# Optimization experiments

Measured on AMD Instinct MI355X. Metric: run time of the kernel, lower is better.

## Reference

```python
import jax, jax.numpy as jnp
import numpy as np

MODEL_DIMS = 2048
BATCH, SEQ = 4, 4096
NFREQ = MODEL_DIMS // 2 + 1  # rfft spectrum length


def setup_inputs() -> dict:
    key = jax.random.key(0)
    k1, k2, k3, k4 = jax.random.split(key, 4)
    x = jax.random.normal(k1, (BATCH, SEQ, MODEL_DIMS), dtype=jnp.float32)
    queries = jax.random.normal(k2, (1, 1, NFREQ), dtype=jnp.float32)
    keyvalues = jax.random.normal(k3, (1, 1, NFREQ), dtype=jnp.float32)
    # torch nn.Linear(model_dims, model_dims, bias=False): weight is [out, in]
    w_out = jax.random.normal(k4, (MODEL_DIMS, MODEL_DIMS), dtype=jnp.float32) * (MODEL_DIMS ** -0.5)
    return {"x": x, "queries": queries, "keyvalues": keyvalues, "w_out": w_out}


def reference(x, queries, keyvalues, w_out):
    # hrr.fft = rfft over feature dim -> complex64 [B, S, NFREQ]
    xhat = jnp.fft.rfft(x, axis=-1)
    q = xhat * queries            # real spectral params broadcast-multiply
    kv = xhat * keyvalues
    kv = jnp.cumsum(kv, axis=1)   # causal prefix sum over sequence
    qv = q * kv
    values_hat = jnp.fft.irfft(qv, n=x.shape[-1], axis=-1)  # back to real [B, S, D]
    # torch Linear: y = x @ W^T
    return jnp.einsum('bsd,ed->bse', values_hat, w_out)
```

## Files before the change

kernel.cpp:

```cpp
#include <hip/hip_runtime.h>
#include <hip/hip_bf16.h>
#include <stdint.h>

#define BATCH 4
#define SEQ   4096
#define DIM   2048
#define NFREQ 1025
#define NCPLX 1024
#define ROWS  (BATCH*SEQ)

#define SCH  16
#define NSC  (SEQ/SCH)
#define NSCG 16
#define NGRP (NSC/NSCG)

#define SPEC_STRIDE 257

typedef __bf16 bf16x8 __attribute__((ext_vector_type(8)));
typedef float  f32x4  __attribute__((ext_vector_type(4)));

__device__ __forceinline__ int drev4(int n) {
  return ((n&3)<<8) | (((n>>2)&3)<<6) | (((n>>4)&3)<<4) | (((n>>6)&3)<<2) | ((n>>8)&3);
}
#define ZI(i) ((i) + ((i)>>4))

__device__ __forceinline__ float2 cmulf(float2 a, float2 b) {
  return make_float2(a.x*b.x - a.y*b.y, a.x*b.y + a.y*b.x);
}

__device__ __forceinline__ unsigned short f2bf(float f) {
  union { float f; unsigned u; } v; v.f = f;
  unsigned r = v.u + 0x7fffu + ((v.u >> 16) & 1u);
  return (unsigned short)(r >> 16);
}
__device__ __forceinline__ unsigned packbf(float2 v) {
  return (unsigned)f2bf(v.x) | ((unsigned)f2bf(v.y) << 16);
}
__device__ __forceinline__ float2 unpackbf(unsigned u) {
  union { unsigned u; float f; } a, b;
  a.u = u << 16; b.u = u & 0xffff0000u;
  return make_float2(a.f, b.f);
}

template<int INV>
__device__ __forceinline__ void fft_stages_tw(float2* z, int tid, const float2* tw1) {
  {
    int b4 = tid*4;
    float2 x0=z[ZI(b4)], x1=z[ZI(b4+1)], x2=z[ZI(b4+2)], x3=z[ZI(b4+3)];
    float2 a = make_float2(x0.x+x2.x, x0.y+x2.y), b = make_float2(x0.x-x2.x, x0.y-x2.y);
    float2 c = make_float2(x1.x+x3.x, x1.y+x3.y), d = make_float2(x1.x-x3.x, x1.y-x3.y);
    z[ZI(b4)]   = make_float2(a.x+c.x, a.y+c.y);
    z[ZI(b4+2)] = make_float2(a.x-c.x, a.y-c.y);
    if (!INV) { z[ZI(b4+1)] = make_float2(b.x+d.y, b.y-d.x);
                z[ZI(b4+3)] = make_float2(b.x-d.y, b.y+d.x); }
    else      { z[ZI(b4+1)] = make_float2(b.x-d.y, b.y+d.x);
                z[ZI(b4+3)] = make_float2(b.x+d.y, b.y-d.x); }
  }
  __syncthreads();
#pragma unroll
  for (int s = 0; s < 4; ++s) {
    const int lq = 2 + 2*s;
    const int q  = 1 << lq;
    int j = tid & (q-1), g = tid >> lq;
    int base = (g << (lq+2)) + j;
    float2 w1 = tw1[s]; if (INV) w1.y = -w1.y;
    float2 w2 = cmulf(w1, w1), w3 = cmulf(w2, w1);
    float2 x0 = z[ZI(base)];
    float2 x1 = cmulf(z[ZI(base+q)],   w1);
    float2 x2 = cmulf(z[ZI(base+2*q)], w2);
    float2 x3 = cmulf(z[ZI(base+3*q)], w3);
    float2 a = make_float2(x0.x+x2.x, x0.y+x2.y), b = make_float2(x0.x-x2.x, x0.y-x2.y);
    float2 c = make_float2(x1.x+x3.x, x1.y+x3.y), d = make_float2(x1.x-x3.x, x1.y-x3.y);
    z[ZI(base)]     = make_float2(a.x+c.x, a.y+c.y);
    z[ZI(base+2*q)] = make_float2(a.x-c.x, a.y-c.y);
    if (!INV) { z[ZI(base+q)]   = make_float2(b.x+d.y, b.y-d.x);
                z[ZI(base+3*q)] = make_float2(b.x-d.y, b.y+d.x); }
    else      { z[ZI(base+q)]   = make_float2(b.x-d.y, b.y+d.x);
                z[ZI(base+3*q)] = make_float2(b.x+d.y, b.y-d.x); }
    __syncthreads();
  }
}

__device__ __forceinline__ void make_tw1(int tid, float2* tw1) {
#pragma unroll
  for (int s = 0; s < 4; ++s) {
    const int lq = 2 + 2*s;
    const int q  = 1 << lq;
    int j = tid & (q-1);
    float ang = -6.2831853071795864769f * (float)j / (float)(4*q);
    float sw, cw; __sincosf(ang, &sw, &cw);
    tw1[s] = make_float2(cw, sw);
  }
}

__global__ __launch_bounds__(256) void fwd_wfft(const float* __restrict__ x,
                                                const float* __restrict__ w,
                                                const float* __restrict__ kvs,
                                                uint4* __restrict__ spec,
                                                float2* __restrict__ partial,
                                                unsigned short* __restrict__ H) {
  __shared__ float2 z[ZI(1023)+2];
  __shared__ __align__(16) unsigned short hrow[2048];
  const int tid = threadIdx.x;

  float2 tw1[4];
  make_tw1(tid, tw1);
  const int kA = tid, kB = tid + 256;
  int id0 = ZI(drev4(2*tid)),     id1 = ZI(drev4(2*tid+1));
  int id2 = ZI(drev4(2*tid+512)), id3 = ZI(drev4(2*tid+513));

  if (blockIdx.x >= BATCH*NSC) {
    const int e = blockIdx.x - BATCH*NSC;
    float swA, cwA, swB, cwB;
    __sincosf(-3.14159265358979323846f * (float)kA / 1024.0f, &swA, &cwA);
    __sincosf(-3.14159265358979323846f * (float)kB / 1024.0f, &swB, &cwB);
    const float* wr = w + (size_t)e * DIM;
    float4 c0 = ((const float4*)wr)[tid];
    float4 c1 = ((const float4*)wr)[tid + 256];
    z[id0] = make_float2(c0.x, c0.y); z[id1] = make_float2(c0.z, c0.w);
    z[id2] = make_float2(c1.x, c1.y); z[id3] = make_float2(c1.z, c1.w);
    __syncthreads();
    fft_stages_tw<0>(z, tid, tw1);
    float2 ZkA = z[ZI(kA)], ZnA = z[ZI((NCPLX - kA) & (NCPLX-1))];
    float2 ZkB = z[ZI(kB)], ZnB = z[ZI(768 - tid)];
    float Er = 0.5f*(ZkA.x + ZnA.x), Ei = 0.5f*(ZkA.y - ZnA.y);
    float dr = 0.5f*(ZkA.x - ZnA.x), di = 0.5f*(ZkA.y + ZnA.y);
    float2 vA  = make_float2( Er + cwA*di + swA*dr,  Ei + swA*di - cwA*dr);
    float2 vAp = make_float2( Er - cwA*di - swA*dr, -Ei + swA*di - cwA*dr);
    float Fr = 0.5f*(ZkB.x + ZnB.x), Fi = 0.5f*(ZkB.y - ZnB.y);
    float er = 0.5f*(ZkB.x - ZnB.x), ei = 0.5f*(ZkB.y + ZnB.y);
    float2 vB  = make_float2( Fr + cwB*ei + swB*er,  Fi + swB*ei - cwB*er);
    float2 vBp = make_float2( Fr - cwB*ei - swB*er, -Fi + swB*ei - cwB*er);
    const float invN = 1.0f/2048.0f, twoN = 2.0f/2048.0f;
    float aA  = (tid == 0) ? invN : twoN;
    hrow[tid]        = f2bf(aA   * vA.x);
    hrow[1024 - tid] = f2bf(aA   * vAp.x);
    hrow[256 + tid]  = f2bf(twoN * vB.x);
    hrow[768 - tid]  = f2bf(twoN * vBp.x);
    if (tid) {
      hrow[1024 + tid] = f2bf(twoN * vA.y);
      hrow[2048 - tid] = f2bf(twoN * vAp.y);
    }
    hrow[1280 + tid] = f2bf(twoN * vB.y);
    hrow[1792 - tid] = f2bf(twoN * vBp.y);
    if (tid == 0) {
      float2 Z5 = z[ZI(512)];
      hrow[512]  = f2bf(twoN * Z5.x);
      hrow[1536] = f2bf(twoN * (-Z5.y));
    }
    __syncthreads();
    ((uint4*)(H + (size_t)e * DIM))[tid] = ((const uint4*)hrow)[tid];
    return;
  }

  const int sc = blockIdx.x & (NSC-1), b = blockIdx.x >> 8;
  float swA, cwA, swB, cwB;
  __sincosf(-3.14159265358979323846f * (float)kA / 1024.0f, &swA, &cwA);
  __sincosf(-3.14159265358979323846f * (float)kB / 1024.0f, &swB, &cwB);

  float2 sA={0,0}, sAp={0,0}, sB={0,0}, sBp={0,0}, s5={0,0};

  const size_t row0 = (size_t)b*SEQ + (size_t)sc*SCH;
  const float* xrow = x + row0*DIM;
  float4 c0 = ((const float4*)xrow)[tid];
  float4 c1 = ((const float4*)xrow)[tid + 256];

  for (int s = 0; s < SCH; ++s) {
    float4 n0f, n1f;
    if (s+1 < SCH) {
      const float* nx = xrow + (size_t)(s+1)*DIM;
      n0f = ((const float4*)nx)[tid]; n1f = ((const float4*)nx)[tid + 256];
    }
    z[id0] = make_float2(c0.x, c0.y); z[id1] = make_float2(c0.z, c0.w);
    z[id2] = make_float2(c1.x, c1.y); z[id3] = make_float2(c1.z, c1.w);
    __syncthreads();
    fft_stages_tw<0>(z, tid, tw1);
    float2 ZkA = z[ZI(kA)], ZnA = z[ZI((NCPLX - kA) & (NCPLX-1))];
    float2 ZkB = z[ZI(kB)], ZnB = z[ZI(768 - tid)];
    float Er = 0.5f*(ZkA.x + ZnA.x), Ei = 0.5f*(ZkA.y - ZnA.y);
    float dr = 0.5f*(ZkA.x - ZnA.x), di = 0.5f*(ZkA.y + ZnA.y);
    float2 vA  = make_float2( Er + cwA*di + swA*dr,  Ei + swA*di - cwA*dr);
    float2 vAp = make_float2( Er - cwA*di - swA*dr, -Ei + swA*di - cwA*dr);
    float Fr = 0.5f*(ZkB.x + ZnB.x), Fi = 0.5f*(ZkB.y - ZnB.y);
    float er = 0.5f*(ZkB.x - ZnB.x), ei = 0.5f*(ZkB.y + ZnB.y);
    float2 vB  = make_float2( Fr + cwB*ei + swB*er,  Fi + swB*ei - cwB*er);
    float2 vBp = make_float2( Fr - cwB*ei - swB*er, -Fi + swB*ei - cwB*er);
    sA.x += vA.x;  sA.y += vA.y;   sAp.x += vAp.x; sAp.y += vAp.y;
    sB.x += vB.x;  sB.y += vB.y;   sBp.x += vBp.x; sBp.y += vBp.y;
    uint4* sprow = spec + (row0 + s) * SPEC_STRIDE;
    sprow[tid] = make_uint4(packbf(vA), packbf(vAp), packbf(vB), packbf(vBp));
    if (tid == 0) {
      float2 Z5 = z[ZI(512)];
      float2 v5 = make_float2(Z5.x, -Z5.y);
      s5.x += v5.x; s5.y += v5.y;
      ((unsigned*)(sprow + 256))[0] = packbf(v5);
    }
    __syncthreads();
    c0 = n0f; c1 = n1f;
  }
  float2* pp = partial + ((size_t)(b*NSC + sc)) * NFREQ;
  float kvA = kvs[kA], kvAp = kvs[NCPLX - kA], kvB = kvs[kB], kvBp = kvs[768 - tid];
  pp[kA]          = make_float2(kvA*sA.x,  kvA*sA.y);
  pp[NCPLX - kA]  = make_float2(kvAp*sAp.x, kvAp*sAp.y);
  pp[kB]          = make_float2(kvB*sB.x,  kvB*sB.y);
  pp[768 - tid]   = make_float2(kvBp*sBp.x, kvBp*sBp.y);
  if (tid == 0) { float kv5 = kvs[512]; pp[512] = make_float2(kv5*s5.x, kv5*s5.y); }
}

__global__ __launch_bounds__(256) void scanA(float2* __restrict__ partial,
                                             float2* __restrict__ gtot) {
  int kc = blockIdx.x % 5, g = (blockIdx.x / 5) % NGRP, b = blockIdx.x / (5*NGRP);
  int k = kc*256 + threadIdx.x;
  if (k >= NFREQ) return;
  float2* p = partial + ((size_t)(b*NSC + g*NSCG)) * NFREQ + k;
  float2 run = {0.f, 0.f};
#pragma unroll
  for (int i = 0; i < NSCG; ++i) {
    float2 t = p[(size_t)i*NFREQ];
    p[(size_t)i*NFREQ] = run;
    run.x += t.x; run.y += t.y;
  }
  gtot[((size_t)(b*NGRP + g)) * NFREQ + k] = run;
}

__global__ __launch_bounds__(256) void inv_fused(const uint4* __restrict__ spec,
                                                 const float* __restrict__ kvs,
                                                 const float* __restrict__ qs_,
                                                 const float2* __restrict__ partial,
                                                 const float2* __restrict__ gtot,
                                                 unsigned short* __restrict__ G) {
  __shared__ __align__(16) unsigned short grow[2][2048];
  const int tid = threadIdx.x;
  const int sc = blockIdx.x & (NSC-1), b = blockIdx.x >> 8;
  const int kA = tid, kB = tid + 256;

  float ksA = kvs[kA], ksAp = kvs[NCPLX - kA], ksB = kvs[kB], ksBp = kvs[768 - tid];
  float qsA = qs_[kA], qsAp = qs_[NCPLX - kA], qsB = qs_[kB], qsBp = qs_[768 - tid];

  const float2* pp = partial + ((size_t)(b*NSC + sc)) * NFREQ;
  float2 CA  = pp[kA], CAp = pp[NCPLX-kA], CB = pp[kB], CBp = pp[768-tid];
  float ks5 = kvs[512], qs5 = qs_[512];
  float2 C5 = pp[512];
  {
    const int g = sc >> 4;
    const float2* gb = gtot + (size_t)b*NGRP*NFREQ;
    for (int gg = 0; gg < g; ++gg) {
      const float2* gr = gb + (size_t)gg*NFREQ;
      float2 a0 = gr[kA], a1 = gr[NCPLX-kA], a2 = gr[kB], a3 = gr[768-tid];
      CA.x += a0.x; CA.y += a0.y;   CAp.x += a1.x; CAp.y += a1.y;
      CB.x += a2.x; CB.y += a2.y;   CBp.x += a3.x; CBp.y += a3.y;
      if (tid == 0) { float2 a5 = gr[512]; C5.x += a5.x; C5.y += a5.y; }
    }
  }

  const size_t row0 = (size_t)b*SEQ + (size_t)sc*SCH;
  const uint4* sprow = spec + row0 * SPEC_STRIDE;
  uint4 sp = sprow[tid];
  unsigned spN = ((const unsigned*)(sprow + 256))[0];

  for (int s = 0; s < SCH; ++s) {
    uint4 spn; unsigned spNn;
    if (s+1 < SCH) {
      const uint4* nr = sprow + (size_t)(s+1) * SPEC_STRIDE;
      spn = nr[tid]; spNn = ((const unsigned*)(nr + 256))[0];
    }
    unsigned short* gw = grow[s & 1];
    float2 vA = unpackbf(sp.x), vAp = unpackbf(sp.y);
    float2 vB = unpackbf(sp.z), vBp = unpackbf(sp.w);
    CA.x  += vA.x*ksA;   CA.y  += vA.y*ksA;
    CAp.x += vAp.x*ksAp; CAp.y += vAp.y*ksAp;
    CB.x  += vB.x*ksB;   CB.y  += vB.y*ksB;
    CBp.x += vBp.x*ksBp; CBp.y += vBp.y*ksBp;
    float2 qvA  = make_float2(qsA *(vA.x*CA.x  - vA.y*CA.y),  qsA *(vA.x*CA.y  + vA.y*CA.x));
    float2 qvAp = make_float2(qsAp*(vAp.x*CAp.x- vAp.y*CAp.y),qsAp*(vAp.x*CAp.y+ vAp.y*CAp.x));
    float2 qvB  = make_float2(qsB *(vB.x*CB.x  - vB.y*CB.y),  qsB *(vB.x*CB.y  + vB.y*CB.x));
    float2 qvBp = make_float2(qsBp*(vBp.x*CBp.x- vBp.y*CBp.y),qsBp*(vBp.x*CBp.y+ vBp.y*CBp.x));
    gw[tid]        = f2bf(qvA.x);
    gw[1024 - tid] = f2bf(qvAp.x);
    gw[256 + tid]  = f2bf(qvB.x);
    gw[768 - tid]  = f2bf(qvBp.x);
    if (tid) {
      gw[1024 + tid] = f2bf(qvA.y);
      gw[2048 - tid] = f2bf(qvAp.y);
    }
    gw[1280 + tid] = f2bf(qvB.y);
    gw[1792 - tid] = f2bf(qvBp.y);
    if (tid == 0) {
      float2 v5 = unpackbf(spN);
      C5.x += v5.x*ks5; C5.y += v5.y*ks5;
      gw[512]  = f2bf(qs5*(v5.x*C5.x - v5.y*C5.y));
      gw[1536] = f2bf(qs5*(v5.x*C5.y + v5.y*C5.x));
    }
    __syncthreads();
    ((uint4*)(G + (row0 + s) * DIM))[tid] = ((const uint4*)gw)[tid];
    sp = spn; spN = spNn;
  }
}

#define NKT (DIM/64)
#define NIT (NKT/2)

#define BAR()  __builtin_amdgcn_s_barrier()
#define VMW(N) do{ asm volatile("s_waitcnt vmcnt(" #N ")" ::: "memory"); __builtin_amdgcn_sched_barrier(0); }while(0)

#define LOADA(B_, MH) do{ _Pragma("unroll") for (int m_=0;m_<4;++m_) _Pragma("unroll") for (int kk_=0;kk_<2;++kk_){ \
    int rA_ = wm*64 + m_*16 + l15; \
    aF[m_][kk_] = *(const bf16x8*)(smem + ((B_)*2+(MH))*16384 + rA_*128 + ((kk_*64 + lhi*16) ^ ((rA_&7)<<4))); } }while(0)

#define LOADB(DST, B_, NH) do{ _Pragma("unroll") for (int n_=0;n_<2;++n_) _Pragma("unroll") for (int kk_=0;kk_<2;++kk_){ \
    int rB_ = wn*32 + n_*16 + l15; \
    DST[n_][kk_] = *(const bf16x8*)(smem + 65536 + ((B_)*2+(NH))*16384 + rB_*128 + ((kk_*64 + lhi*16) ^ ((rB_&7)<<4))); } }while(0)

#define MM(MH, NH, BF) do{ __builtin_amdgcn_s_setprio(1); \
    _Pragma("unroll") for (int kk_=0;kk_<2;++kk_) _Pragma("unroll") for (int m_=0;m_<4;++m_) _Pragma("unroll") for (int n_=0;n_<2;++n_) \
      acc[MH][NH][m_][n_] = __builtin_amdgcn_mfma_f32_16x16x32_bf16(aF[m_][kk_], BF[n_][kk_], acc[MH][NH][m_][n_], 0, 0, 0); \
    __builtin_amdgcn_s_setprio(0); }while(0)

#define STAGEH(REG, B_, H_, GP, ROW0, KT) do{ _Pragma("unroll") for (int c_=0;c_<2;++c_){ \
    int ci_ = c_*512 + tid; int r_ = ci_>>3, sl_ = ci_&7; \
    const unsigned short* sp_ = (GP) + (size_t)((ROW0) + (H_)*128 + r_)*DIM + (KT) + ((sl_ ^ (r_&7))*8); \
    __builtin_amdgcn_global_load_lds((const __attribute__((address_space(1))) void*)sp_, \
      (__attribute__((address_space(3))) void*)(smem + (REG) + ((B_)*2+(H_))*16384 + ci_*16), 16, 0, 0); } }while(0)

__global__ __launch_bounds__(512, 2) void gemm256(const unsigned short* __restrict__ A,
                                                  const unsigned short* __restrict__ B,
                                                  float* __restrict__ C) {
  __shared__ __align__(16) char smem[131072];
  const int tid = threadIdx.x;
  const int lane = tid & 63;
  const int wid  = tid >> 6;
  const int wm = wid >> 2, wn = wid & 3;
  const int l15 = lane & 15, lhi = lane >> 4;

  const int xj = blockIdx.x & 7, tt = blockIdx.x >> 3;
  const int bm = xj * 8 + (tt >> 3), bn = tt & 7;
  const int m0 = bm * 256, n0 = bn * 256;

  f32x4 acc[2][2][4][2] = {};
  bf16x8 aF[4][2], bF0[2][2], bF1[2][2];

  STAGEH(0,     0,0, A, m0, 0);  STAGEH(65536, 0,0, B, n0, 0);
  STAGEH(65536, 0,1, B, n0, 0);  STAGEH(0,     0,1, A, m0, 0);
  STAGEH(0,     1,0, A, m0, 64); STAGEH(65536, 1,0, B, n0, 64);
  STAGEH(65536, 1,1, B, n0, 64); STAGEH(0,     1,1, A, m0, 64);
  VMW(8);
  BAR();

#pragma unroll 1
  for (int j = 0; j < NIT-1; ++j) {
    const int kA = (2*j+2)*64, kB = (2*j+3)*64;
    LOADA(0,0); LOADB(bF0, 0,0);
    BAR(); MM(0,0,bF0); BAR();
    LOADB(bF1, 0,1);
    STAGEH(0, 0,0, A, m0, kA); STAGEH(65536, 0,0, B, n0, kA);
    BAR(); MM(0,1,bF1); BAR();
    LOADA(0,1);
    STAGEH(65536, 0,1, B, n0, kA);
    BAR(); MM(1,0,bF0); BAR();
    STAGEH(0, 0,1, A, m0, kA);
    BAR(); MM(1,1,bF1); VMW(8); BAR();
    LOADA(1,0); LOADB(bF0, 1,0);
    BAR(); MM(0,0,bF0); BAR();
    LOADB(bF1, 1,1);
    STAGEH(0, 1,0, A, m0, kB); STAGEH(65536, 1,0, B, n0, kB);
    BAR(); MM(0,1,bF1); BAR();
    LOADA(1,1);
    STAGEH(65536, 1,1, B, n0, kB);
    BAR(); MM(1,0,bF0); BAR();
    STAGEH(0, 1,1, A, m0, kB);
    BAR(); MM(1,1,bF1); VMW(8); BAR();
  }
  LOADA(0,0); LOADB(bF0, 0,0);
  BAR(); MM(0,0,bF0); BAR();
  LOADB(bF1, 0,1);
  BAR(); MM(0,1,bF1); BAR();
  LOADA(0,1);
  BAR(); MM(1,0,bF0); BAR();
  BAR(); MM(1,1,bF1); VMW(0); BAR();
  LOADA(1,0); LOADB(bF0, 1,0);
  BAR(); MM(0,0,bF0); BAR();
  LOADB(bF1, 1,1);
  BAR(); MM(0,1,bF1); BAR();
  LOADA(1,1);
  BAR(); MM(1,0,bF0); BAR();
  BAR(); MM(1,1,bF1); BAR();

  const int crow = lhi * 4;
#pragma unroll
  for (int mh = 0; mh < 2; ++mh)
#pragma unroll
    for (int nh = 0; nh < 2; ++nh)
#pragma unroll
      for (int m_ = 0; m_ < 4; ++m_)
#pragma unroll
        for (int n_ = 0; n_ < 2; ++n_) {
          float* cp = C + (size_t)(m0 + mh*128 + wm*64 + m_*16 + crow) * DIM
                        + (n0 + nh*128 + wn*32 + n_*16 + l15);
#pragma unroll
          for (int j2 = 0; j2 < 4; ++j2)
            cp[(size_t)j2 * DIM] = acc[mh][nh][m_][n_][j2];
        }
}

extern "C" void kernel_launch(void* const* d_in, const int* in_sizes, int n_in,
                              void* d_out, int out_size, void* d_ws, size_t ws_size,
                              hipStream_t stream) {
  const float* x    = (const float*)d_in[0];
  const float* qry  = (const float*)d_in[1];
  const float* kvs  = (const float*)d_in[2];
  const float* wout = (const float*)d_in[3];
  float* out = (float*)d_out;

  char* ws = (char*)d_ws;
  size_t off = 0;
  uint4* spec = (uint4*)(ws + off);
  off += (size_t)ROWS * SPEC_STRIDE * sizeof(uint4);
  off = (off + 255) & ~(size_t)255;
  unsigned short* G = (unsigned short*)(ws + off);
  off += (size_t)ROWS * DIM * sizeof(unsigned short);
  off = (off + 255) & ~(size_t)255;
  unsigned short* H = (unsigned short*)(ws + off);
  off += (size_t)DIM * DIM * sizeof(unsigned short);
  off = (off + 255) & ~(size_t)255;
  float2* partial = (float2*)(ws + off);
  off += (size_t)BATCH * NSC * NFREQ * sizeof(float2);
  off = (off + 255) & ~(size_t)255;
  float2* gtot = (float2*)(ws + off);
  off += (size_t)BATCH * NGRP * NFREQ * sizeof(float2);

  hipLaunchKernelGGL(fwd_wfft,  dim3(BATCH*NSC + DIM),   dim3(256), 0, stream, x, wout, kvs, spec, partial, H);
  hipLaunchKernelGGL(scanA,     dim3(BATCH*NGRP*5),      dim3(256), 0, stream, partial, gtot);
  hipLaunchKernelGGL(inv_fused, dim3(BATCH*NSC),         dim3(256), 0, stream, spec, kvs, qry, partial, gtot, G);
  hipLaunchKernelGGL(gemm256,   dim3((ROWS/256)*(DIM/256)), dim3(512), 0, stream, G, H, out);
}
```

Measured before the change: 223.3 us.

## Restructure GEMM main loop to halve barriers and re-stagger A/B staging

Reworks the software-pipelined bf16 GEMM loop so each phase issues two MFMA blocks between a single barrier pair instead of one, halving the number of workgroup barriers. The last A sub-tile of each K slice is now staged one phase later, interleaved with the next slice's loads, and the vmcnt waits change from 8 to 6 to match the new count of in-flight global-to-LDS copies. The aim is less barrier stall and better overlap of global loads with matrix math, at the cost of a more delicate LDS reuse schedule that could race if the wait counts are wrong.

New measurement: 226.6 us. No clear change (+1.5%).

```diff
diff --git a/kernel.cpp b/kernel.cpp
--- a/kernel.cpp
+++ b/kernel.cpp
@@ -342,48 +342,35 @@
   STAGEH(0,     0,0, A, m0, 0);  STAGEH(65536, 0,0, B, n0, 0);
   STAGEH(65536, 0,1, B, n0, 0);  STAGEH(0,     0,1, A, m0, 0);
   STAGEH(0,     1,0, A, m0, 64); STAGEH(65536, 1,0, B, n0, 64);
-  STAGEH(65536, 1,1, B, n0, 64); STAGEH(0,     1,1, A, m0, 64);
-  VMW(8);
+  STAGEH(65536, 1,1, B, n0, 64);
+  VMW(6);
   BAR();
 
 #pragma unroll 1
   for (int j = 0; j < NIT-1; ++j) {
-    const int kA = (2*j+2)*64, kB = (2*j+3)*64;
-    LOADA(0,0); LOADB(bF0, 0,0);
-    BAR(); MM(0,0,bF0); BAR();
-    LOADB(bF1, 0,1);
-    STAGEH(0, 0,0, A, m0, kA); STAGEH(65536, 0,0, B, n0, kA);
-    BAR(); MM(0,1,bF1); BAR();
+    const int k1 = (2*j+1)*64, k2 = (2*j+2)*64, k3 = (2*j+3)*64;
+    LOADA(0,0); LOADB(bF0, 0,0); LOADB(bF1, 0,1);
+    STAGEH(0, 1,1, A, m0, k1);
+    BAR(); MM(0,0,bF0); MM(0,1,bF1); BAR();
     LOADA(0,1);
-    STAGEH(65536, 0,1, B, n0, kA);
-    BAR(); MM(1,0,bF0); BAR();
-    STAGEH(0, 0,1, A, m0, kA);
-    BAR(); MM(1,1,bF1); VMW(8); BAR();
-    LOADA(1,0); LOADB(bF0, 1,0);
-    BAR(); MM(0,0,bF0); BAR();
-    LOADB(bF1, 1,1);
-    STAGEH(0, 1,0, A, m0, kB); STAGEH(65536, 1,0, B, n0, kB);
-    BAR(); MM(0,1,bF1); BAR();
+    STAGEH(0, 0,0, A, m0, k2); STAGEH(65536, 0,0, B, n0, k2); STAGEH(65536, 0,1, B, n0, k2);
+    BAR(); MM(1,0,bF0); MM(1,1,bF1); VMW(6); BAR();
+    LOADA(1,0); LOADB(bF0, 1,0); LOADB(bF1, 1,1);
+    STAGEH(0, 0,1, A, m0, k2);
+    BAR(); MM(0,0,bF0); MM(0,1,bF1); BAR();
     LOADA(1,1);
-    STAGEH(65536, 1,1, B, n0, kB);
-    BAR(); MM(1,0,bF0); BAR();
-    STAGEH(0, 1,1, A, m0, kB);
-    BAR(); MM(1,1,bF1); VMW(8); BAR();
-  }
-  LOADA(0,0); LOADB(bF0, 0,0);
-  BAR(); MM(0,0,bF0); BAR();
-  LOADB(bF1, 0,1);
-  BAR(); MM(0,1,bF1); BAR();
+    STAGEH(0, 1,0, A, m0, k3); STAGEH(65536, 1,0, B, n0, k3); STAGEH(65536, 1,1, B, n0, k3);
+    BAR(); MM(1,0,bF0); MM(1,1,bF1); VMW(6); BAR();
+  }
+  LOADA(0,0); LOADB(bF0, 0,0); LOADB(bF1, 0,1);
+  STAGEH(0, 1,1, A, m0, 31*64);
+  BAR(); MM(0,0,bF0); MM(0,1,bF1); BAR();
   LOADA(0,1);
-  BAR(); MM(1,0,bF0); BAR();
-  BAR(); MM(1,1,bF1); VMW(0); BAR();
-  LOADA(1,0); LOADB(bF0, 1,0);
-  BAR(); MM(0,0,bF0); BAR();
-  LOADB(bF1, 1,1);
-  BAR(); MM(0,1,bF1); BAR();
+  BAR(); MM(1,0,bF0); MM(1,1,bF1); VMW(0); BAR();
+  LOADA(1,0); LOADB(bF0, 1,0); LOADB(bF1, 1,1);
+  BAR(); MM(0,0,bF0); MM(0,1,bF1); BAR();
   LOADA(1,1);
-  BAR(); MM(1,0,bF0); BAR();
-  BAR(); MM(1,1,bF1); BAR();
+  BAR(); MM(1,0,bF0); MM(1,1,bF1); BAR();
 
   const int crow = lhi * 4;
 #pragma unroll
```
